# Optimization experiments

Measured on AMD Instinct MI355X. Metric: run time of the kernel, lower is better.

## Reference

```python
import jax, jax.numpy as jnp
import numpy as np

DECAY = 0.99


def setup_inputs() -> dict:
    key = jax.random.key(0)
    k1, k2, k3 = jax.random.split(key, 3)
    B, D, H, W = 16, 128, 32, 32
    K = 8192
    z_e = jax.random.normal(k1, (B, D, H, W), dtype=jnp.float32)
    codebook = jax.random.normal(k2, (K, D), dtype=jnp.float32)
    ema_count = jnp.ones((K,), dtype=jnp.float32)
    ema_weight = codebook  # buffer initialized as codebook.clone()
    return {"z_e": z_e, "codebook": codebook, "ema_count": ema_count, "ema_weight": ema_weight}


def reference(z_e, codebook, ema_count, ema_weight):
    B, D, H, W = z_e.shape
    K = codebook.shape[0]
    # (B,D,H,W) -> (N,D)
    z_flat = z_e.transpose(0, 2, 3, 1).reshape(-1, D)
    # squared L2 distances: ||z||^2 - 2 z.C^T + ||C||^2  -> (N,K)
    dist = (
        jnp.sum(z_flat * z_flat, axis=1, keepdims=True)
        - 2.0 * (z_flat @ codebook.T)
        + jnp.sum(codebook * codebook, axis=1)[None, :]
    )
    indices = jnp.argmin(dist, axis=1)  # (N,)
    z_q = codebook[indices].reshape(B, H, W, D).transpose(0, 3, 1, 2)
    # EMA codebook update (training path, no grad)
    counts = jax.ops.segment_sum(jnp.ones_like(indices, dtype=jnp.float32), indices, num_segments=K)
    dw = jax.ops.segment_sum(z_flat, indices, num_segments=K)  # (K,D)
    new_count = ema_count * DECAY + (1.0 - DECAY) * counts
    new_weight = ema_weight * DECAY + (1.0 - DECAY) * dw
    new_codebook = new_weight / jnp.maximum(new_count, 1.0)[:, None]
    # straight-through estimator
    z_q_st = z_e + jax.lax.stop_gradient(z_q - z_e)
    return (z_q_st, indices.reshape(B, H, W), new_codebook, new_count, new_weight)
```

## Files before the change

### kernel.cpp

```cpp
#include <hip/hip_runtime.h>

#define D 128
#define HW 1024
#define NROWS 16384
#define K 8192
#define NU 32

#define OUT0 0
#define OUT1 2097152
#define OUT2 2113536
#define OUT3 3162112
#define OUT4 3170304

typedef __attribute__((ext_vector_type(8))) _Float16 half8;
typedef __attribute__((ext_vector_type(16))) float f32x16;
typedef unsigned short u16;
typedef unsigned long long u64;

__device__ __forceinline__ void gld16(const u16* gsrc, u16* ldst) {
    __builtin_amdgcn_global_load_lds(
        (const __attribute__((address_space(1))) unsigned int*)gsrc,
        (__attribute__((address_space(3))) unsigned int*)ldst,
        16, 0, 0);
}

__global__ __launch_bounds__(256) void k_prep(const float* __restrict__ cb,
                                              const float* __restrict__ z_e,
                                              u16* __restrict__ Bg,
                                              float* __restrict__ cnorm,
                                              u16* __restrict__ Ah, u16* __restrict__ Al,
                                              u64* __restrict__ packed,
                                              float* __restrict__ counts,
                                              float* __restrict__ dw) {
    const int tid = threadIdx.x;
    if (blockIdx.x < 512) {
        int kk = tid & 15;
        int k = blockIdx.x * 16 + (tid >> 4);
        const float* src = cb + (size_t)k * D + kk * 8;
        half8 h, l;
        float s = 0.f;
#pragma unroll
        for (int j = 0; j < 8; ++j) {
            float v = src[j];
            s += v * v;
            _Float16 hv = (_Float16)v;
            _Float16 lv = (_Float16)(v - (float)hv);
            h[j] = hv;
            l[j] = lv;
        }
        int g = k >> 6, col = k & 63;
        size_t offH = (size_t)g * 16384 + ((size_t)kk * 64 + col) * 8;
        *(half8*)((_Float16*)Bg + offH) = h;
        *(half8*)((_Float16*)Bg + offH + 8192) = l;
#pragma unroll
        for (int off = 8; off > 0; off >>= 1) s += __shfl_down(s, off);
        if (kk == 0) cnorm[k] = s;
        float4 z4 = {0.f, 0.f, 0.f, 0.f};
        size_t zi = ((size_t)blockIdx.x * 256 + tid) * 8;
        *(float4*)(dw + zi) = z4;
        *(float4*)(dw + zi + 4) = z4;
    } else {
        int gid = (blockIdx.x - 512) * 256 + tid;
        int n  = gid & (NROWS - 1);
        int kk = gid >> 14;
        int b = n >> 10, hw = n & 1023;
        const float* src = z_e + ((size_t)b * D + kk * 8) * HW + hw;
        half8 h, l;
#pragma unroll
        for (int j = 0; j < 8; ++j) {
            float v = src[(size_t)j * HW];
            _Float16 hv = (_Float16)v;
            _Float16 lv = (_Float16)(v - (float)hv);
            h[j] = hv;
            l[j] = lv;
        }
        int rg = n >> 7, band = (n >> 5) & 3, row = n & 31;
        size_t off = (((((size_t)rg * 4 + band) * 8 + (kk >> 1)) * 2 + (kk & 1)) * 32 + row) * 8;
        *(half8*)(Ah + off) = h;
        *(half8*)(Al + off) = l;
        if (kk == 0) {
            packed[n] = ~0ull;
            if (n < K) counts[n] = 0.f;
        }
    }
}

__global__ __launch_bounds__(512, 4) void k_argmin_mfma(
        const u16* __restrict__ Ahg, const u16* __restrict__ Alg,
        const u16* __restrict__ Bg,
        const float* __restrict__ cnorm, u64* __restrict__ packed) {
    __shared__ u16 lds[2][16384];

    const int tid = threadIdx.x;
    const int ln  = tid & 63;
    const int l31 = ln & 31;
    const int lh  = ln >> 5;
    const int wv  = tid >> 6;
    const int wy  = wv & 3;
    const int wx  = wv >> 2;

    const int rg = blockIdx.x >> 2;
    const int k0 = (blockIdx.x & 3) * 2048;
    const int g0 = k0 >> 6;

    half8 Ah[8], Al[8];
#pragma unroll
    for (int ks = 0; ks < 8; ++ks) {
        size_t off = ((((size_t)(rg * 4 + wy) * 8 + ks) * 2 + lh) * 32 + l31) * 8;
        Ah[ks] = *(const half8*)((const _Float16*)Ahg + off);
        Al[ks] = *(const half8*)((const _Float16*)Alg + off);
    }

    {
        const u16* src = Bg + (size_t)g0 * 16384;
#pragma unroll
        for (int r = 0; r < 4; ++r)
            gld16(src + ((size_t)r * 512 + tid) * 8, lds[0] + (r * 512 + tid) * 8);
    }

    float minv[16];
    int   mini[16];
#pragma unroll
    for (int r = 0; r < 16; ++r) { minv[r] = INFINITY; mini[r] = 0; }

#pragma unroll 1
    for (int u = 0; u < NU; ++u) {
        const u16* buf = lds[u & 1];
        const int c0 = k0 + u * 64 + wx * 32 + l31;

        float cn0 = cnorm[c0];

        if (u + 1 < NU) {
            const u16* src = Bg + (size_t)(g0 + u + 1) * 16384;
            u16* dst = lds[(u + 1) & 1];
#pragma unroll
            for (int r = 0; r < 4; ++r)
                gld16(src + ((size_t)r * 512 + tid) * 8, dst + (r * 512 + tid) * 8);
            asm volatile("s_waitcnt vmcnt(4)" ::: "memory");
        } else {
            asm volatile("s_waitcnt vmcnt(0)" ::: "memory");
        }
        asm volatile("s_barrier" ::: "memory");

        f32x16 acc = {};
        const _Float16* bh = (const _Float16*)buf;
        const _Float16* bl = bh + 8192;

#pragma unroll
        for (int ks = 0; ks < 8; ++ks) {
            const int bo = ((ks * 2 + lh) * 64 + wx * 32 + l31) * 8;
            half8 b0 = *(const half8*)(bl + bo);
            acc = __builtin_amdgcn_mfma_f32_32x32x16_f16(Ah[ks], b0, acc, 0, 0, 0);
        }
#pragma unroll
        for (int ks = 0; ks < 8; ++ks) {
            const int bo = ((ks * 2 + lh) * 64 + wx * 32 + l31) * 8;
            half8 b0 = *(const half8*)(bh + bo);
            acc = __builtin_amdgcn_mfma_f32_32x32x16_f16(Ah[ks], b0, acc, 0, 0, 0);
            acc = __builtin_amdgcn_mfma_f32_32x32x16_f16(Al[ks], b0, acc, 0, 0, 0);
        }

#pragma unroll
        for (int r = 0; r < 16; ++r) {
            float d0 = fmaf(-2.0f, acc[r], cn0);
            if (d0 < minv[r]) { minv[r] = d0; mini[r] = c0; }
        }
        asm volatile("s_barrier" ::: "memory");
    }

#pragma unroll
    for (int r = 0; r < 16; ++r) {
        float v = minv[r];
        int ix = mini[r];
#pragma unroll
        for (int off = 1; off < 32; off <<= 1) {
            float v2 = __shfl_xor(v, off);
            int i2 = __shfl_xor(ix, off);
            if (v2 < v || (v2 == v && i2 < ix)) { v = v2; ix = i2; }
        }
        if (l31 == 0) {
            int row = rg * 128 + wy * 32 + 4 * lh + (r & 3) + 8 * (r >> 2);
            unsigned int uenc = __float_as_uint(v);
            uenc = (uenc & 0x80000000u) ? ~uenc : (uenc | 0x80000000u);
            u64 pk = ((u64)uenc << 13) | (u64)(unsigned)ix;
            atomicMin(&packed[row], pk);
        }
    }
}

__global__ __launch_bounds__(256) void k_epilogue(const float* __restrict__ z_e,
                                                  const float* __restrict__ cb,
                                                  const u64* __restrict__ packed,
                                                  float* __restrict__ out0,
                                                  float* __restrict__ out1,
                                                  float* __restrict__ counts,
                                                  float* __restrict__ dw) {
    __shared__ int idxS[64];
    const int tid = threadIdx.x;
    const int n0 = blockIdx.x * 64;
    const int bb = n0 >> 10, p0 = n0 & 1023;

    if (tid < 64) {
        int ix = (int)(packed[n0 + tid] & 0x1FFFull);
        idxS[tid] = ix;
        out1[n0 + tid] = (float)ix;
        atomicAdd(&counts[ix], 1.0f);
    }
    __syncthreads();

    const float* zb = z_e + (size_t)bb * (D * HW) + p0;
    float* ob = out0 + (size_t)bb * (D * HW) + p0;

    for (int i = tid; i < 64 * D; i += 256) {
        int d = i >> 6, r = i & 63;
        float z = zb[(size_t)d * HW + r];
        float c = cb[(size_t)idxS[r] * D + d];
        ob[(size_t)d * HW + r] = z + (c - z);
    }
    for (int i = tid; i < 64 * D; i += 256) {
        int r = i >> 7, d = i & 127;
        atomicAdd(&dw[(size_t)idxS[r] * D + d], zb[(size_t)d * HW + r]);
    }
}

__global__ __launch_bounds__(256) void k_final(const float* __restrict__ ema_count,
                                               const float* __restrict__ ema_weight,
                                               float* __restrict__ out2,
                                               float* __restrict__ out3,
                                               float* __restrict__ out4) {
    int gid = blockIdx.x * 256 + threadIdx.x;
    int k = gid >> 7, d = gid & 127;
    float cnt_raw = out3[k];
    float dw_raw = out4[gid];
    __syncthreads();
    float nc = 0.99f * ema_count[k] + 0.01f * cnt_raw;
    float nw = 0.99f * ema_weight[gid] + 0.01f * dw_raw;
    out4[gid] = nw;
    out2[gid] = nw / fmaxf(nc, 1.0f);
    if (d == 0) out3[k] = nc;
}

extern "C" void kernel_launch(void* const* d_in, const int* in_sizes, int n_in,
                              void* d_out, int out_size, void* d_ws, size_t ws_size,
                              hipStream_t stream) {
    const float* z_e        = (const float*)d_in[0];
    const float* cb         = (const float*)d_in[1];
    const float* ema_count  = (const float*)d_in[2];
    const float* ema_weight = (const float*)d_in[3];
    float* out = (float*)d_out;

    float* cnorm = (float*)d_ws;
    u64* packed = (u64*)((char*)d_ws + K * 4);

    u16* Ahg = (u16*)(out + OUT0);
    u16* Alg = Ahg + (size_t)NROWS * D;
    u16* Bg  = (u16*)(out + OUT2);

    k_prep       <<<1536,          256, 0, stream>>>(cb, z_e, Bg, cnorm, Ahg, Alg,
                                                     packed, out + OUT3, out + OUT4);
    k_argmin_mfma<<<512,           512, 0, stream>>>(Ahg, Alg, Bg, cnorm, packed);
    k_epilogue   <<<NROWS / 64,    256, 0, stream>>>(z_e, cb, packed,
                                                     out + OUT0, out + OUT1,
                                                     out + OUT3, out + OUT4);
    k_final      <<<(K * D) / 256, 256, 0, stream>>>(ema_count, ema_weight,
                                                     out + OUT2, out + OUT3, out + OUT4);
}
```

Baseline: 211.7 us.

## Double row tile per wave in argmin GEMM and stage low-half A in LDS

```diff
diff --git a/kernel.cpp b/kernel.cpp
--- a/kernel.cpp
+++ b/kernel.cpp
@@ -85,11 +85,14 @@
     }
 }
 
-__global__ __launch_bounds__(512, 4) void k_argmin_mfma(
+__global__ __launch_bounds__(512, 2) void k_argmin_mfma(
         const u16* __restrict__ Ahg, const u16* __restrict__ Alg,
         const u16* __restrict__ Bg,
         const float* __restrict__ cnorm, u64* __restrict__ packed) {
-    __shared__ u16 lds[2][16384];
+    extern __shared__ u16 smem[];
+    u16* Bb0 = smem;
+    u16* Bb1 = smem + 16384;
+    u16* AlS = smem + 32768;
 
     const int tid = threadIdx.x;
     const int ln  = tid & 63;
@@ -102,37 +105,43 @@
     const int rg = blockIdx.x >> 2;
     const int k0 = (blockIdx.x & 3) * 2048;
     const int g0 = k0 >> 6;
-
-    half8 Ah[8], Al[8];
+    const int t0 = wy * 2;
+
+    half8 Ah0[8], Ah1[8];
 #pragma unroll
     for (int ks = 0; ks < 8; ++ks) {
-        size_t off = ((((size_t)(rg * 4 + wy) * 8 + ks) * 2 + lh) * 32 + l31) * 8;
-        Ah[ks] = *(const half8*)((const _Float16*)Ahg + off);
-        Al[ks] = *(const half8*)((const _Float16*)Alg + off);
+        size_t o0 = ((((size_t)(rg * 8 + t0)     * 8 + ks) * 2 + lh) * 32 + l31) * 8;
+        size_t o1 = ((((size_t)(rg * 8 + t0 + 1) * 8 + ks) * 2 + lh) * 32 + l31) * 8;
+        Ah0[ks] = *(const half8*)((const _Float16*)Ahg + o0);
+        Ah1[ks] = *(const half8*)((const _Float16*)Ahg + o1);
     }
 
     {
-        const u16* src = Bg + (size_t)g0 * 16384;
+        const u16* srcA = Alg + (size_t)rg * 32768;
+#pragma unroll
+        for (int r = 0; r < 8; ++r)
+            gld16(srcA + ((size_t)r * 512 + tid) * 8, AlS + (r * 512 + tid) * 8);
+        const u16* srcB = Bg + (size_t)g0 * 16384;
 #pragma unroll
         for (int r = 0; r < 4; ++r)
-            gld16(src + ((size_t)r * 512 + tid) * 8, lds[0] + (r * 512 + tid) * 8);
-    }
-
-    float minv[16];
-    int   mini[16];
-#pragma unroll
-    for (int r = 0; r < 16; ++r) { minv[r] = INFINITY; mini[r] = 0; }
+            gld16(srcB + ((size_t)r * 512 + tid) * 8, Bb0 + (r * 512 + tid) * 8);
+    }
+
+    float minv[32];
+    int   mini[32];
+#pragma unroll
+    for (int r = 0; r < 32; ++r) { minv[r] = INFINITY; mini[r] = 0; }
 
 #pragma unroll 1
     for (int u = 0; u < NU; ++u) {
-        const u16* buf = lds[u & 1];
+        const u16* buf = (u & 1) ? Bb1 : Bb0;
         const int c0 = k0 + u * 64 + wx * 32 + l31;
 
         float cn0 = cnorm[c0];
 
         if (u + 1 < NU) {
             const u16* src = Bg + (size_t)(g0 + u + 1) * 16384;
-            u16* dst = lds[(u + 1) & 1];
+            u16* dst = (u & 1) ? Bb0 : Bb1;
 #pragma unroll
             for (int r = 0; r < 4; ++r)
                 gld16(src + ((size_t)r * 512 + tid) * 8, dst + (r * 512 + tid) * 8);
@@ -142,48 +151,61 @@
         }
         asm volatile("s_barrier" ::: "memory");
 
-        f32x16 acc = {};
+        f32x16 acc0 = {}, acc1 = {};
         const _Float16* bh = (const _Float16*)buf;
         const _Float16* bl = bh + 8192;
-
+        const _Float16* al = (const _Float16*)AlS;
+
+        __builtin_amdgcn_s_setprio(1);
 #pragma unroll
         for (int ks = 0; ks < 8; ++ks) {
             const int bo = ((ks * 2 + lh) * 64 + wx * 32 + l31) * 8;
             half8 b0 = *(const half8*)(bl + bo);
-            acc = __builtin_amdgcn_mfma_f32_32x32x16_f16(Ah[ks], b0, acc, 0, 0, 0);
+            acc0 = __builtin_amdgcn_mfma_f32_32x32x16_f16(Ah0[ks], b0, acc0, 0, 0, 0);
+            acc1 = __builtin_amdgcn_mfma_f32_32x32x16_f16(Ah1[ks], b0, acc1, 0, 0, 0);
         }
 #pragma unroll
         for (int ks = 0; ks < 8; ++ks) {
             const int bo = ((ks * 2 + lh) * 64 + wx * 32 + l31) * 8;
             half8 b0 = *(const half8*)(bh + bo);
-            acc = __builtin_amdgcn_mfma_f32_32x32x16_f16(Ah[ks], b0, acc, 0, 0, 0);
-            acc = __builtin_amdgcn_mfma_f32_32x32x16_f16(Al[ks], b0, acc, 0, 0, 0);
-        }
+            half8 a0 = *(const half8*)(al + ((((t0)     * 8 + ks) * 2 + lh) * 32 + l31) * 8);
+            half8 a1 = *(const half8*)(al + ((((t0 + 1) * 8 + ks) * 2 + lh) * 32 + l31) * 8);
+            acc0 = __builtin_amdgcn_mfma_f32_32x32x16_f16(Ah0[ks], b0, acc0, 0, 0, 0);
+            acc1 = __builtin_amdgcn_mfma_f32_32x32x16_f16(Ah1[ks], b0, acc1, 0, 0, 0);
+            acc0 = __builtin_amdgcn_mfma_f32_32x32x16_f16(a0, b0, acc0, 0, 0, 0);
+            acc1 = __builtin_amdgcn_mfma_f32_32x32x16_f16(a1, b0, acc1, 0, 0, 0);
+        }
+        __builtin_amdgcn_s_setprio(0);
 
 #pragma unroll
         for (int r = 0; r < 16; ++r) {
-            float d0 = fmaf(-2.0f, acc[r], cn0);
-            if (d0 < minv[r]) { minv[r] = d0; mini[r] = c0; }
+            float d0 = fmaf(-2.0f, acc0[r], cn0);
+            float d1 = fmaf(-2.0f, acc1[r], cn0);
+            if (d0 < minv[r])      { minv[r]      = d0; mini[r]      = c0; }
+            if (d1 < minv[16 + r]) { minv[16 + r] = d1; mini[16 + r] = c0; }
         }
         asm volatile("s_barrier" ::: "memory");
     }
 
 #pragma unroll
-    for (int r = 0; r < 16; ++r) {
-        float v = minv[r];
-        int ix = mini[r];
-#pragma unroll
-        for (int off = 1; off < 32; off <<= 1) {
-            float v2 = __shfl_xor(v, off);
-            int i2 = __shfl_xor(ix, off);
-            if (v2 < v || (v2 == v && i2 < ix)) { v = v2; ix = i2; }
-        }
-        if (l31 == 0) {
-            int row = rg * 128 + wy * 32 + 4 * lh + (r & 3) + 8 * (r >> 2);
-            unsigned int uenc = __float_as_uint(v);
-            uenc = (uenc & 0x80000000u) ? ~uenc : (uenc | 0x80000000u);
-            u64 pk = ((u64)uenc << 13) | (u64)(unsigned)ix;
-            atomicMin(&packed[row], pk);
+    for (int t = 0; t < 2; ++t) {
+#pragma unroll
+        for (int r = 0; r < 16; ++r) {
+            float v = minv[t * 16 + r];
+            int ix = mini[t * 16 + r];
+#pragma unroll
+            for (int off = 1; off < 32; off <<= 1) {
+                float v2 = __shfl_xor(v, off);
+                int i2 = __shfl_xor(ix, off);
+                if (v2 < v || (v2 == v && i2 < ix)) { v = v2; ix = i2; }
+            }
+            if (l31 == 0) {
+                int row = rg * 256 + (t0 + t) * 32 + 4 * lh + (r & 3) + 8 * (r >> 2);
+                unsigned int uenc = __float_as_uint(v);
+                uenc = (uenc & 0x80000000u) ? ~uenc : (uenc | 0x80000000u);
+                u64 pk = ((u64)uenc << 13) | (u64)(unsigned)ix;
+                atomicMin(&packed[row], pk);
+            }
         }
     }
 }
@@ -256,12 +278,19 @@
     u16* Alg = Ahg + (size_t)NROWS * D;
     u16* Bg  = (u16*)(out + OUT2);
 
-    k_prep       <<<1536,          256, 0, stream>>>(cb, z_e, Bg, cnorm, Ahg, Alg,
-                                                     packed, out + OUT3, out + OUT4);
-    k_argmin_mfma<<<512,           512, 0, stream>>>(Ahg, Alg, Bg, cnorm, packed);
-    k_epilogue   <<<NROWS / 64,    256, 0, stream>>>(z_e, cb, packed,
-                                                     out + OUT0, out + OUT1,
-                                                     out + OUT3, out + OUT4);
-    k_final      <<<(K * D) / 256, 256, 0, stream>>>(ema_count, ema_weight,
-                                                     out + OUT2, out + OUT3, out + OUT4);
-}
+    static bool attr_done = false;
+    if (!attr_done) {
+        hipFuncSetAttribute(reinterpret_cast<const void*>(k_argmin_mfma),
+                            hipFuncAttributeMaxDynamicSharedMemorySize, 131072);
+        attr_done = true;
+    }
+
+    k_prep       <<<1536,          256, 0,      stream>>>(cb, z_e, Bg, cnorm, Ahg, Alg,
+                                                          packed, out + OUT3, out + OUT4);
+    k_argmin_mfma<<<256,           512, 131072, stream>>>(Ahg, Alg, Bg, cnorm, packed);
+    k_epilogue   <<<NROWS / 64,    256, 0,      stream>>>(z_e, cb, packed,
+                                                          out + OUT0, out + OUT1,
+                                                          out + OUT3, out + OUT4);
+    k_final      <<<(K * D) / 256, 256, 0,      stream>>>(ema_count, ema_weight,
+                                                          out + OUT2, out + OUT3, out + OUT4);
+}
```

Measured after the change: 215.7 us. No clear change (+1.9%).

## Fuse z_e fp16 split into argmin kernel and stage z tile in LDS for epilogue

Applied to the files above, without the earlier changes.

```diff
diff --git a/kernel.cpp b/kernel.cpp
--- a/kernel.cpp
+++ b/kernel.cpp
@@ -25,68 +25,44 @@
 }
 
 __global__ __launch_bounds__(256) void k_prep(const float* __restrict__ cb,
-                                              const float* __restrict__ z_e,
                                               u16* __restrict__ Bg,
                                               float* __restrict__ cnorm,
-                                              u16* __restrict__ Ah, u16* __restrict__ Al,
                                               u64* __restrict__ packed,
                                               float* __restrict__ counts,
                                               float* __restrict__ dw) {
     const int tid = threadIdx.x;
-    if (blockIdx.x < 512) {
-        int kk = tid & 15;
-        int k = blockIdx.x * 16 + (tid >> 4);
-        const float* src = cb + (size_t)k * D + kk * 8;
-        half8 h, l;
-        float s = 0.f;
-#pragma unroll
-        for (int j = 0; j < 8; ++j) {
-            float v = src[j];
-            s += v * v;
-            _Float16 hv = (_Float16)v;
-            _Float16 lv = (_Float16)(v - (float)hv);
-            h[j] = hv;
-            l[j] = lv;
-        }
-        int g = k >> 6, col = k & 63;
-        size_t offH = (size_t)g * 16384 + ((size_t)kk * 64 + col) * 8;
-        *(half8*)((_Float16*)Bg + offH) = h;
-        *(half8*)((_Float16*)Bg + offH + 8192) = l;
-#pragma unroll
-        for (int off = 8; off > 0; off >>= 1) s += __shfl_down(s, off);
-        if (kk == 0) cnorm[k] = s;
-        float4 z4 = {0.f, 0.f, 0.f, 0.f};
-        size_t zi = ((size_t)blockIdx.x * 256 + tid) * 8;
-        *(float4*)(dw + zi) = z4;
-        *(float4*)(dw + zi + 4) = z4;
-    } else {
-        int gid = (blockIdx.x - 512) * 256 + tid;
-        int n  = gid & (NROWS - 1);
-        int kk = gid >> 14;
-        int b = n >> 10, hw = n & 1023;
-        const float* src = z_e + ((size_t)b * D + kk * 8) * HW + hw;
-        half8 h, l;
-#pragma unroll
-        for (int j = 0; j < 8; ++j) {
-            float v = src[(size_t)j * HW];
-            _Float16 hv = (_Float16)v;
-            _Float16 lv = (_Float16)(v - (float)hv);
-            h[j] = hv;
-            l[j] = lv;
-        }
-        int rg = n >> 7, band = (n >> 5) & 3, row = n & 31;
-        size_t off = (((((size_t)rg * 4 + band) * 8 + (kk >> 1)) * 2 + (kk & 1)) * 32 + row) * 8;
-        *(half8*)(Ah + off) = h;
-        *(half8*)(Al + off) = l;
-        if (kk == 0) {
-            packed[n] = ~0ull;
-            if (n < K) counts[n] = 0.f;
-        }
-    }
+    int kk = tid & 15;
+    int k = blockIdx.x * 16 + (tid >> 4);
+    const float* src = cb + (size_t)k * D + kk * 8;
+    half8 h, l;
+    float s = 0.f;
+#pragma unroll
+    for (int j = 0; j < 8; ++j) {
+        float v = src[j];
+        s += v * v;
+        _Float16 hv = (_Float16)v;
+        _Float16 lv = (_Float16)(v - (float)hv);
+        h[j] = hv;
+        l[j] = lv;
+    }
+    int g = k >> 6, col = k & 63;
+    size_t offH = (size_t)g * 16384 + ((size_t)kk * 64 + col) * 8;
+    *(half8*)((_Float16*)Bg + offH) = h;
+    *(half8*)((_Float16*)Bg + offH + 8192) = l;
+#pragma unroll
+    for (int off = 8; off > 0; off >>= 1) s += __shfl_down(s, off);
+    if (kk == 0) cnorm[k] = s;
+    float4 z4 = {0.f, 0.f, 0.f, 0.f};
+    size_t zi = ((size_t)blockIdx.x * 256 + tid) * 8;
+    *(float4*)(dw + zi) = z4;
+    *(float4*)(dw + zi + 4) = z4;
+    int gid = blockIdx.x * 256 + tid;
+    if (gid < NROWS) packed[gid] = ~0ull;
+    if (gid < K) counts[gid] = 0.f;
 }
 
 __global__ __launch_bounds__(512, 4) void k_argmin_mfma(
-        const u16* __restrict__ Ahg, const u16* __restrict__ Alg,
+        const float* __restrict__ z_e,
         const u16* __restrict__ Bg,
         const float* __restrict__ cnorm, u64* __restrict__ packed) {
     __shared__ u16 lds[2][16384];
@@ -103,12 +79,21 @@
     const int k0 = (blockIdx.x & 3) * 2048;
     const int g0 = k0 >> 6;
 
+    const int row = (rg * 4 + wy) * 32 + l31;
+    const float* zrow = z_e + ((size_t)(row >> 10)) * (D * HW) + (row & 1023);
     half8 Ah[8], Al[8];
 #pragma unroll
     for (int ks = 0; ks < 8; ++ks) {
-        size_t off = ((((size_t)(rg * 4 + wy) * 8 + ks) * 2 + lh) * 32 + l31) * 8;
-        Ah[ks] = *(const half8*)((const _Float16*)Ahg + off);
-        Al[ks] = *(const half8*)((const _Float16*)Alg + off);
+        half8 h, l;
+#pragma unroll
+        for (int j = 0; j < 8; ++j) {
+            float v = zrow[(size_t)(ks * 16 + lh * 8 + j) * HW];
+            _Float16 hv = (_Float16)v;
+            h[j] = hv;
+            l[j] = (_Float16)(v - (float)hv);
+        }
+        Ah[ks] = h;
+        Al[ks] = l;
     }
 
     {
@@ -179,11 +164,11 @@
             if (v2 < v || (v2 == v && i2 < ix)) { v = v2; ix = i2; }
         }
         if (l31 == 0) {
-            int row = rg * 128 + wy * 32 + 4 * lh + (r & 3) + 8 * (r >> 2);
+            int orow = rg * 128 + wy * 32 + 4 * lh + (r & 3) + 8 * (r >> 2);
             unsigned int uenc = __float_as_uint(v);
             uenc = (uenc & 0x80000000u) ? ~uenc : (uenc | 0x80000000u);
             u64 pk = ((u64)uenc << 13) | (u64)(unsigned)ix;
-            atomicMin(&packed[row], pk);
+            atomicMin(&packed[orow], pk);
         }
     }
 }
@@ -195,6 +180,7 @@
                                                   float* __restrict__ out1,
                                                   float* __restrict__ counts,
                                                   float* __restrict__ dw) {
+    __shared__ float zS[128][65];
     __shared__ int idxS[64];
     const int tid = threadIdx.x;
     const int n0 = blockIdx.x * 64;
@@ -214,12 +200,14 @@
     for (int i = tid; i < 64 * D; i += 256) {
         int d = i >> 6, r = i & 63;
         float z = zb[(size_t)d * HW + r];
+        zS[d][r] = z;
         float c = cb[(size_t)idxS[r] * D + d];
         ob[(size_t)d * HW + r] = z + (c - z);
     }
+    __syncthreads();
     for (int i = tid; i < 64 * D; i += 256) {
         int r = i >> 7, d = i & 127;
-        atomicAdd(&dw[(size_t)idxS[r] * D + d], zb[(size_t)d * HW + r]);
+        atomicAdd(&dw[(size_t)idxS[r] * D + d], zS[d][r]);
     }
 }
 
@@ -252,13 +240,11 @@
     float* cnorm = (float*)d_ws;
     u64* packed = (u64*)((char*)d_ws + K * 4);
 
-    u16* Ahg = (u16*)(out + OUT0);
-    u16* Alg = Ahg + (size_t)NROWS * D;
-    u16* Bg  = (u16*)(out + OUT2);
-
-    k_prep       <<<1536,          256, 0, stream>>>(cb, z_e, Bg, cnorm, Ahg, Alg,
+    u16* Bg = (u16*)(out + OUT2);
+
+    k_prep       <<<512,           256, 0, stream>>>(cb, Bg, cnorm,
                                                      packed, out + OUT3, out + OUT4);
-    k_argmin_mfma<<<512,           512, 0, stream>>>(Ahg, Alg, Bg, cnorm, packed);
+    k_argmin_mfma<<<512,           512, 0, stream>>>(z_e, Bg, cnorm, packed);
     k_epilogue   <<<NROWS / 64,    256, 0, stream>>>(z_e, cb, packed,
                                                      out + OUT0, out + OUT1,
                                                      out + OUT3, out + OUT4);
```

Result: faster. 200.6 us (-5.2%).
